# Kernel tuning notes

Measured on AMD Instinct MI355X. Metric: run time of the kernel, lower is better.

## Reference

```python
import jax, jax.numpy as jnp
import numpy as np

N_HEADS = 16


def setup_inputs() -> dict:
    key = jax.random.key(0)
    ks = jax.random.split(key, 4)
    B, S, E = 4, 2048, 1024
    x = jax.random.normal(ks[0], (B, S, E), dtype=jnp.float32)
    w_attn = jax.random.normal(ks[1], (E, 3 * E), dtype=jnp.float32) * 0.02
    b_attn = jnp.zeros((3 * E,), dtype=jnp.float32)
    w_proj = jax.random.normal(ks[2], (E, E), dtype=jnp.float32) * 0.02
    b_proj = jnp.zeros((E,), dtype=jnp.float32)
    return {"x": x, "w_attn": w_attn, "b_attn": b_attn, "w_proj": w_proj, "b_proj": b_proj}


def reference(x, w_attn, b_attn, w_proj, b_proj):
    B, S, E = x.shape
    H = N_HEADS
    D = E // H
    # fused QKV projection (Conv1D: x @ W + b)
    qkv = x @ w_attn + b_attn                     # [B, S, 3E]
    q, k, v = jnp.split(qkv, 3, axis=-1)          # each [B, S, E]
    q = q.reshape(B, S, H, D).transpose(0, 2, 1, 3)  # [B, H, S, D]
    k = k.reshape(B, S, H, D).transpose(0, 2, 1, 3)
    v = v.reshape(B, S, H, D).transpose(0, 2, 1, 3)
    # scaled QK^T
    scores = jnp.einsum('bhqd,bhkd->bhqk', q, k) / jnp.sqrt(jnp.asarray(D, dtype=x.dtype))
    # causal mask via where with dtype-min fill (matches torch.where(c_m, w, finfo.min))
    causal = jnp.tril(jnp.ones((S, S), dtype=bool))  # [S, S]
    scores = jnp.where(causal[None, None, :, :], scores, jnp.finfo(scores.dtype).min)
    attn = jax.nn.softmax(scores, axis=-1)        # [B, H, S, S]
    o = jnp.einsum('bhqk,bhkd->bhqd', attn, v)    # [B, H, S, D]
    o = o.transpose(0, 2, 1, 3).reshape(B, S, E)  # merge heads
    return o @ w_proj + b_proj                    # output projection
```

## Files before the change

kernel.cpp:

```cpp
#include <hip/hip_runtime.h>
#include <stdint.h>


typedef __bf16 bf16;
typedef __bf16 bf16x4 __attribute__((ext_vector_type(4)));
typedef __bf16 bf16x8 __attribute__((ext_vector_type(8)));
typedef float  f32x4  __attribute__((ext_vector_type(4)));

#define DEV __device__ __forceinline__

DEV void async_copy16(bf16* lds, const bf16* g) {
  __builtin_amdgcn_global_load_lds(
      (__attribute__((address_space(1))) void*)(uintptr_t)g,
      (__attribute__((address_space(3))) void*)(uint32_t)(uintptr_t)lds,
      16, 0, 0);
}

__global__ __launch_bounds__(256) void cast_x_kernel(const float* __restrict__ in,
                                                     bf16* __restrict__ out, int n4) {
  int i = blockIdx.x * blockDim.x + threadIdx.x;
  int stride = gridDim.x * blockDim.x;
  for (; i < n4; i += stride) {
    float4 v = ((const float4*)in)[i];
    bf16x4 o = { (bf16)v.x, (bf16)v.y, (bf16)v.z, (bf16)v.w };
    *(bf16x4*)(out + (size_t)i * 4) = o;
  }
}

__global__ __launch_bounds__(256) void transpose_cast_kernel(const float* __restrict__ W,
                                                             bf16* __restrict__ Wt,
                                                             int Kd, int Nd) {
  __shared__ alignas(16) bf16 T[64 * 80];
  const int t = threadIdx.x;
  const int n0 = blockIdx.x * 64;
  const int k0 = blockIdx.y * 64;
#pragma unroll
  for (int i = 0; i < 4; ++i) {
    int idx = t + i * 256;
    int r  = idx >> 4;
    int c4 = (idx & 15) * 4;
    float4 v = *(const float4*)(W + (size_t)(k0 + r) * Nd + n0 + c4);
    bf16x4 o = { (bf16)v.x, (bf16)v.y, (bf16)v.z, (bf16)v.w };
    *(bf16x4*)(&T[r * 80 + c4]) = o;
  }
  __syncthreads();
#pragma unroll
  for (int i = 0; i < 2; ++i) {
    int idx = t + i * 256;
    int n = idx >> 3;
    int c = idx & 7;
    bf16x8 o;
#pragma unroll
    for (int j = 0; j < 8; ++j) o[j] = T[(c * 8 + j) * 80 + n];
    *(bf16x8*)(Wt + (size_t)(n0 + n) * Kd + k0 + c * 8) = o;
  }
}

template <typename OutT, bool FUSE_VT>
__global__ __launch_bounds__(512, 4) void gemm256_kernel(const bf16* __restrict__ A,
                                                         const bf16* __restrict__ Bt,
                                                         const float* __restrict__ bias,
                                                         OutT* __restrict__ C,
                                                         bf16* __restrict__ vtout,
                                                         int M, int N, int K,
                                                         float qscale, int qcols,
                                                         int nbx) {
  __shared__ alignas(16) char smem[73728];
  auto As = (bf16(*)[256 * 32])smem;
  auto Bs = (bf16(*)[128 * 32])(smem + 49152);

  const int tid  = threadIdx.x;
  const int lane = tid & 63;
  const int w    = tid >> 6;
  const int wm = w >> 1, wn = w & 1;
  const int l15 = lane & 15, l16 = lane >> 4;

  const int nwg = (int)gridDim.x;
  const int cpx = nwg >> 3;
  const int swz = ((int)blockIdx.x & 7) * cpx + ((int)blockIdx.x >> 3);
  const int m0 = (swz / nbx) * 256;
  const int n0 = (swz % nbx) * 128;

  const int c0  = w * 64 + lane;
  const int rA0 = c0 >> 2, sA0 = c0 & 3;
  const int rA1 = rA0 + 128;
  const bf16* srcA0 = A  + (size_t)(m0 + rA0) * K + 8 * (sA0 ^ ((rA0 >> 1) & 3));
  const bf16* srcA1 = A  + (size_t)(m0 + rA1) * K + 8 * (sA0 ^ ((rA1 >> 1) & 3));
  const bf16* srcB  = Bt + (size_t)(n0 + rA0) * K + 8 * (sA0 ^ ((rA0 >> 1) & 3));

#define STAGE_TILE(buf, kt)                                       \
  {                                                               \
    const int k0_ = (kt) * 32;                                    \
    async_copy16(&As[buf][(w * 64) * 8],         srcA0 + k0_);    \
    async_copy16(&As[buf][(512 + w * 64) * 8],   srcA1 + k0_);    \
    async_copy16(&Bs[buf][(w * 64) * 8],         srcB  + k0_);    \
  }

  f32x4 acc[4][4];
  f32x4 zf = {0.f, 0.f, 0.f, 0.f};
#pragma unroll
  for (int i = 0; i < 4; ++i)
#pragma unroll
    for (int j = 0; j < 4; ++j) acc[i][j] = zf;

  const int KT = K >> 5;
  STAGE_TILE(0, 0)
  STAGE_TILE(1, 1)

  const int soff = 8 * (l16 ^ ((l15 >> 1) & 3));

  int bufc = 0;
  int bufs = 2;
  for (int kt = 0; kt < KT; ++kt) {
    if (kt < KT - 1) { asm volatile("s_waitcnt vmcnt(3)" ::: "memory"); }
    else             { asm volatile("s_waitcnt vmcnt(0)" ::: "memory"); }
    __builtin_amdgcn_s_barrier();
    asm volatile("" ::: "memory");
    if (kt + 2 < KT) STAGE_TILE(bufs, kt + 2)

    bf16x8 bfr[4], afr[4];
#pragma unroll
    for (int n = 0; n < 4; ++n) {
      int rb = wn * 64 + n * 16 + l15;
      bfr[n] = *(const bf16x8*)(&Bs[bufc][rb * 32 + soff]);
    }
#pragma unroll
    for (int m = 0; m < 4; ++m) {
      int ra = wm * 64 + m * 16 + l15;
      afr[m] = *(const bf16x8*)(&As[bufc][ra * 32 + soff]);
    }
    __builtin_amdgcn_s_setprio(1);
#pragma unroll
    for (int m = 0; m < 4; ++m)
#pragma unroll
      for (int n = 0; n < 4; ++n)
        acc[m][n] = __builtin_amdgcn_mfma_f32_16x16x32_bf16(afr[m], bfr[n], acc[m][n], 0, 0, 0);
    __builtin_amdgcn_s_setprio(0);
    asm volatile("" ::: "memory");
    bufc = (bufc == 2) ? 0 : bufc + 1;
    bufs = (bufs == 2) ? 0 : bufs + 1;
  }

  if (FUSE_VT && n0 >= 2048) {
    __syncthreads();
    bf16* T = (bf16*)smem;
#pragma unroll
    for (int n = 0; n < 4; ++n) {
      int c = wn * 64 + n * 16 + l15;
      float bb = bias[n0 + c];
#pragma unroll
      for (int m = 0; m < 4; ++m) {
        int r0_ = wm * 64 + m * 16 + l16 * 4;
        int key0 = r0_ & 63;
        int pos0 = (key0 & 32) | (((key0 >> 2) & 3) << 3) | (((key0 >> 4) & 1) << 2);
        int rp = (r0_ & ~63) | pos0;
        bf16x4 q = { (bf16)(acc[m][n][0] + bb), (bf16)(acc[m][n][1] + bb),
                     (bf16)(acc[m][n][2] + bb), (bf16)(acc[m][n][3] + bb) };
        *(bf16x4*)(&T[c * 264 + rp]) = q;
      }
    }
    __syncthreads();
    const int b_  = m0 >> 11;
    const int s0_ = m0 & 2047;
    const int ck  = tid & 31;
#pragma unroll
    for (int pass = 0; pass < 8; ++pass) {
      int c = pass * 16 + (tid >> 5);
      int colg = n0 + c - 2048;
      int hh = colg >> 6, d = colg & 63;
      bf16x8 v = *(const bf16x8*)(&T[c * 264 + ck * 8]);
      *(bf16x8*)(vtout + ((size_t)(b_ * 16 + hh) * 64 + d) * 2048 + s0_ + ck * 8) = v;
    }
    return;
  }
#pragma unroll
  for (int n = 0; n < 4; ++n) {
    int col = n0 + wn * 64 + n * 16 + l15;
    float bb = bias[col];
    float sc2 = (col < qcols) ? qscale : 1.0f;
#pragma unroll
    for (int m = 0; m < 4; ++m) {
#pragma unroll
      for (int reg = 0; reg < 4; ++reg) {
        int row = m0 + wm * 64 + m * 16 + l16 * 4 + reg;
        C[(size_t)row * N + col] = (OutT)((acc[m][n][reg] + bb) * sc2);
      }
    }
  }
#undef STAGE_TILE
}

template <typename OutT>
__global__ __launch_bounds__(256, 4) void gemm128_kernel(const bf16* __restrict__ A,
                                                         const bf16* __restrict__ Bt,
                                                         const float* __restrict__ bias,
                                                         OutT* __restrict__ C,
                                                         int M, int N, int K,
                                                         int nbx) {
  __shared__ alignas(16) char smem[49152];
  auto As = (bf16(*)[128 * 32])smem;
  auto Bs = (bf16(*)[128 * 32])(smem + 24576);

  const int tid  = threadIdx.x;
  const int lane = tid & 63;
  const int w    = tid >> 6;
  const int wm = w >> 1, wn = w & 1;
  const int l15 = lane & 15, l16 = lane >> 4;

  const int nwg = (int)gridDim.x;
  const int cpx = nwg >> 3;
  const int swz = ((int)blockIdx.x & 7) * cpx + ((int)blockIdx.x >> 3);
  const int m0 = (swz / nbx) * 128;
  const int n0 = (swz % nbx) * 128;

  const int r0_ = tid >> 2, s0c = tid & 3;
  const int r1_ = r0_ + 64;
  const bf16* srcA0 = A  + (size_t)(m0 + r0_) * K + 8 * (s0c ^ ((r0_ >> 1) & 3));
  const bf16* srcA1 = A  + (size_t)(m0 + r1_) * K + 8 * (s0c ^ ((r1_ >> 1) & 3));
  const bf16* srcB0 = Bt + (size_t)(n0 + r0_) * K + 8 * (s0c ^ ((r0_ >> 1) & 3));
  const bf16* srcB1 = Bt + (size_t)(n0 + r1_) * K + 8 * (s0c ^ ((r1_ >> 1) & 3));

#define STAGE_TILE(buf, kt)                                         \
  {                                                                 \
    const int k0_ = (kt) * 32;                                      \
    async_copy16(&As[buf][(w * 64) * 8],         srcA0 + k0_);      \
    async_copy16(&As[buf][(256 + w * 64) * 8],   srcA1 + k0_);      \
    async_copy16(&Bs[buf][(w * 64) * 8],         srcB0 + k0_);      \
    async_copy16(&Bs[buf][(256 + w * 64) * 8],   srcB1 + k0_);      \
  }

  f32x4 acc[4][4];
  f32x4 zf = {0.f, 0.f, 0.f, 0.f};
#pragma unroll
  for (int i = 0; i < 4; ++i)
#pragma unroll
    for (int j = 0; j < 4; ++j) acc[i][j] = zf;

  const int KT = K >> 5;
  STAGE_TILE(0, 0)
  STAGE_TILE(1, 1)

  const int soff = 8 * (l16 ^ ((l15 >> 1) & 3));

  int bufc = 0;
  int bufs = 2;
  for (int kt = 0; kt < KT; ++kt) {
    if (kt < KT - 1) { asm volatile("s_waitcnt vmcnt(4)" ::: "memory"); }
    else             { asm volatile("s_waitcnt vmcnt(0)" ::: "memory"); }
    __builtin_amdgcn_s_barrier();
    asm volatile("" ::: "memory");
    if (kt + 2 < KT) STAGE_TILE(bufs, kt + 2)

    bf16x8 bfr[4], afr[4];
#pragma unroll
    for (int n = 0; n < 4; ++n) {
      int rb = wn * 64 + n * 16 + l15;
      bfr[n] = *(const bf16x8*)(&Bs[bufc][rb * 32 + soff]);
    }
#pragma unroll
    for (int m = 0; m < 4; ++m) {
      int ra = wm * 64 + m * 16 + l15;
      afr[m] = *(const bf16x8*)(&As[bufc][ra * 32 + soff]);
    }
    __builtin_amdgcn_s_setprio(1);
#pragma unroll
    for (int m = 0; m < 4; ++m)
#pragma unroll
      for (int n = 0; n < 4; ++n)
        acc[m][n] = __builtin_amdgcn_mfma_f32_16x16x32_bf16(afr[m], bfr[n], acc[m][n], 0, 0, 0);
    __builtin_amdgcn_s_setprio(0);
    asm volatile("" ::: "memory");
    bufc = (bufc == 2) ? 0 : bufc + 1;
    bufs = (bufs == 2) ? 0 : bufs + 1;
  }

#pragma unroll
  for (int n = 0; n < 4; ++n) {
    int col = n0 + wn * 64 + n * 16 + l15;
    float bb = bias[col];
#pragma unroll
    for (int m = 0; m < 4; ++m) {
#pragma unroll
      for (int reg = 0; reg < 4; ++reg) {
        int row = m0 + wm * 64 + m * 16 + l16 * 4 + reg;
        C[(size_t)row * N + col] = (OutT)(acc[m][n][reg] + bb);
      }
    }
  }
#undef STAGE_TILE
}

__global__ __launch_bounds__(512, 4) void flash_kernel(const bf16* __restrict__ qkv,
                                                       const bf16* __restrict__ vt,
                                                       bf16* __restrict__ obuf) {
  constexpr int S = 2048, E3 = 3072;
  __shared__ alignas(16) bf16 Ks[2][64 * 64];
  __shared__ alignas(16) bf16 Vs[2][64 * 64];

  const int tid  = threadIdx.x;
  const int lane = tid & 63;
  const int w    = tid >> 6;
  const int i   = (int)blockIdx.x;
  const int bh  = ((i >> 6) << 3) | (i & 7);
  const int bx  = (i >> 3) & 7;
  const int b = bh >> 4, h = bh & 15;
  const int l15 = lane & 15, l16 = lane >> 4;

  const int sr  = w * 8 + (lane >> 3);
  const int scc = lane & 7;
  const bf16* kstage = qkv + (size_t)(b * S + sr) * E3 + 1024 + h * 64 + 8 * (scc ^ (sr & 7));
  const bf16* vstage = vt + (size_t)(bh * 64 + sr) * S + 8 * (scc ^ (sr & 7));

  const int xsw = l15 & 7;
  const uint32_t rdA = (uint32_t)(l15 * 128 + 16 * (l16 ^ xsw));
  const uint32_t rdB = (uint32_t)(l15 * 128 + 16 * ((4 + l16) ^ xsw));

#define KV_STAGE(buf, kv0_)                                        \
  {                                                                \
    async_copy16(Ks[buf] + w * 512, kstage + (size_t)(kv0_) * E3); \
    async_copy16(Vs[buf] + w * 512, vstage + (kv0_));              \
  }

  for (int half = 0; half < 2; ++half) {
    const int t = half ? (15 - bx) : bx;
    const int q0 = t * 128;
    const int wq0 = q0 + w * 16;
    const int nsteps = 2 * t + 2;

    KV_STAGE(0, 0)

    bf16x8 qf[2];
    {
      const bf16* qbase = qkv + (size_t)(b * S + wq0 + l15) * E3 + h * 64;
#pragma unroll
      for (int dk = 0; dk < 2; ++dk)
        qf[dk] = *(const bf16x8*)(qbase + (dk * 4 + l16) * 8);
    }

    float lstate = 0.f;
    f32x4 oacc[4];
    f32x4 zf = {0.f, 0.f, 0.f, 0.f};
#pragma unroll
    for (int i2 = 0; i2 < 4; ++i2) oacc[i2] = zf;

    __syncthreads();

#define FLASH_STEP(CUR, STEPIDX)                                                  \
    {                                                                             \
      const int kv0 = (STEPIDX) * 64;                                             \
      if ((STEPIDX) + 1 < nsteps) KV_STAGE((CUR) ^ 1, kv0 + 64)                   \
      if (kv0 <= wq0 + 15) {                     \
        f32x4 sv[4];                                                              \
        _Pragma("unroll")                                                         \
        for (int kf = 0; kf < 4; ++kf) sv[kf] = zf;                               \
        __builtin_amdgcn_s_setprio(1);                                            \
        _Pragma("unroll")                                                         \
        for (int kf = 0; kf < 4; ++kf) {                                          \
          bf16x8 k0 = *(const bf16x8*)((const char*)Ks[CUR] + rdA + kf * 2048);   \
          sv[kf] = __builtin_amdgcn_mfma_f32_16x16x32_bf16(k0, qf[0], sv[kf], 0, 0, 0); \
          bf16x8 k1 = *(const bf16x8*)((const char*)Ks[CUR] + rdB + kf * 2048);   \
          sv[kf] = __builtin_amdgcn_mfma_f32_16x16x32_bf16(k1, qf[1], sv[kf], 0, 0, 0); \
        }                                                                         \
        __builtin_amdgcn_s_setprio(0);                                            \
        if (kv0 + 63 > wq0) {     \
          const int qrow_ = wq0 + l15;                                            \
          _Pragma("unroll")                                                       \
          for (int kf = 0; kf < 4; ++kf)                                          \
            _Pragma("unroll")                                                     \
            for (int reg = 0; reg < 4; ++reg) {                                   \
              int key = kv0 + kf * 16 + l16 * 4 + reg;                            \
              if (key > qrow_) sv[kf][reg] = -1e30f;                              \
            }                                                                     \
        }                                                                         \
        float rsum = 0.f;                                                         \
        _Pragma("unroll")                                                         \
        for (int kf = 0; kf < 4; ++kf)                                            \
          _Pragma("unroll")                                                       \
          for (int reg = 0; reg < 4; ++reg) {                                     \
            float p = __builtin_amdgcn_exp2f(sv[kf][reg]);                        \
            sv[kf][reg] = p;                                                      \
            rsum += p;                                                            \
          }                                                                       \
        rsum += __shfl_xor(rsum, 16);                                             \
        rsum += __shfl_xor(rsum, 32);                                             \
        lstate += rsum;                                                           \
             \
        bf16x8 pb[2];                                                             \
        _Pragma("unroll")                                                         \
        for (int kc = 0; kc < 2; ++kc) {                                          \
          bf16x8 tq;                                                              \
          tq[0] = (bf16)sv[2 * kc][0];  tq[1] = (bf16)sv[2 * kc][1];              \
          tq[2] = (bf16)sv[2 * kc][2];  tq[3] = (bf16)sv[2 * kc][3];              \
          tq[4] = (bf16)sv[2 * kc + 1][0]; tq[5] = (bf16)sv[2 * kc + 1][1];       \
          tq[6] = (bf16)sv[2 * kc + 1][2]; tq[7] = (bf16)sv[2 * kc + 1][3];       \
          pb[kc] = tq;                                                            \
        }                                                                         \
        __builtin_amdgcn_s_setprio(1);                                            \
        _Pragma("unroll")                                                         \
        for (int nf = 0; nf < 4; ++nf) {                                          \
          bf16x8 vf0 = *(const bf16x8*)((const char*)Vs[CUR] + rdA + nf * 2048);  \
          oacc[nf] = __builtin_amdgcn_mfma_f32_16x16x32_bf16(vf0, pb[0], oacc[nf], 0, 0, 0); \
          bf16x8 vf1 = *(const bf16x8*)((const char*)Vs[CUR] + rdB + nf * 2048);  \
          oacc[nf] = __builtin_amdgcn_mfma_f32_16x16x32_bf16(vf1, pb[1], oacc[nf], 0, 0, 0); \
        }                                                                         \
        __builtin_amdgcn_s_setprio(0);                                            \
      }                                                                           \
      __syncthreads();          \
    }

    for (int step = 0; step < nsteps; step += 2) {
      FLASH_STEP(0, step)
      FLASH_STEP(1, step + 1)
    }
#undef FLASH_STEP

    float inv = 1.0f / lstate;
    int qrow = wq0 + l15;
#pragma unroll
    for (int nf = 0; nf < 4; ++nf) {
      bf16x4 o4 = { (bf16)(oacc[nf][0] * inv), (bf16)(oacc[nf][1] * inv),
                    (bf16)(oacc[nf][2] * inv), (bf16)(oacc[nf][3] * inv) };
      *(bf16x4*)(obuf + (size_t)(b * S + qrow) * 1024 + h * 64 + nf * 16 + l16 * 4) = o4;
    }
  }
#undef KV_STAGE
}

extern "C" void kernel_launch(void* const* d_in, const int* in_sizes, int n_in,
                              void* d_out, int out_size, void* d_ws, size_t ws_size,
                              hipStream_t stream) {
  (void)in_sizes; (void)n_in; (void)out_size; (void)ws_size;
  const float* x      = (const float*)d_in[0];
  const float* w_attn = (const float*)d_in[1];
  const float* b_attn = (const float*)d_in[2];
  const float* w_proj = (const float*)d_in[3];
  const float* b_proj = (const float*)d_in[4];
  float* out = (float*)d_out;

  char* ws = (char*)d_ws;
  bf16* xb  = (bf16*)(ws + 0);
  bf16* wat = (bf16*)(ws + 16777216);
  bf16* wpt = (bf16*)(ws + 23068672);
  bf16* qkv = (bf16*)(ws + 25165824);
  bf16* vt  = (bf16*)(ws + 75497472);
  bf16* ob  = (bf16*)(ws + 92274688);

  const float QSCALE = 0.18033688011112042f;

  cast_x_kernel<<<2048, 256, 0, stream>>>(x, xb, 8192 * 1024 / 4);
  transpose_cast_kernel<<<dim3(48, 16), 256, 0, stream>>>(w_attn, wat, 1024, 3072);
  transpose_cast_kernel<<<dim3(16, 16), 256, 0, stream>>>(w_proj, wpt, 1024, 1024);
  gemm256_kernel<bf16, true><<<768, 512, 0, stream>>>(xb, wat, b_attn, qkv, vt,
                                                      8192, 3072, 1024, QSCALE, 1024, 24);
  flash_kernel<<<512, 512, 0, stream>>>(qkv, vt, ob);
  gemm128_kernel<float><<<512, 256, 0, stream>>>(ob, wpt, b_proj, out,
                                                 8192, 1024, 1024, 8);
}
```

Measured before the change: 146.3 us.

## Switch flash attention to 32x32x16 MFMA with split-KV warp pairs

The flash kernel now uses 32x32x16 bf16 MFMA tiles instead of 16x16x32. Each pair of waves shares a 32-row query block, and each wave of the pair handles one 32-key half of every 64-key tile. The two partial outputs and row sums are combined through new LDS buffers after an extra barrier. The V-transpose permutation in the QKV GEMM epilogue is changed to match the new P register layout expected by the larger MFMA. The aim is fewer MFMA issues and LDS fragment loads per FLOP. In exchange, LDS use rises by about 33 KB and a reduction step is added, which may lower occupancy at 4 blocks per CU.

```diff
diff --git a/kernel.cpp b/kernel.cpp
--- a/kernel.cpp
+++ b/kernel.cpp
@@ -6,6 +6,7 @@
 typedef __bf16 bf16x4 __attribute__((ext_vector_type(4)));
 typedef __bf16 bf16x8 __attribute__((ext_vector_type(8)));
 typedef float  f32x4  __attribute__((ext_vector_type(4)));
+typedef float  f32x16 __attribute__((ext_vector_type(16)));
 
 #define DEV __device__ __forceinline__
 
@@ -152,7 +153,7 @@
       for (int m = 0; m < 4; ++m) {
         int r0_ = wm * 64 + m * 16 + l16 * 4;
         int key0 = r0_ & 63;
-        int pos0 = (key0 & 32) | (((key0 >> 2) & 3) << 3) | (((key0 >> 4) & 1) << 2);
+        int pos0 = (key0 & 0x30) | ((key0 & 8) >> 1) | ((key0 & 4) << 1);
         int rp = (r0_ & ~63) | pos0;
         bf16x4 q = { (bf16)(acc[m][n][0] + bb), (bf16)(acc[m][n][1] + bb),
                      (bf16)(acc[m][n][2] + bb), (bf16)(acc[m][n][3] + bb) };
@@ -296,24 +297,37 @@
   constexpr int S = 2048, E3 = 3072;
   __shared__ alignas(16) bf16 Ks[2][64 * 64];
   __shared__ alignas(16) bf16 Vs[2][64 * 64];
+  __shared__ alignas(16) float Ms[4][32][64];
+  __shared__ float Ls[4][32];
 
   const int tid  = threadIdx.x;
   const int lane = tid & 63;
   const int w    = tid >> 6;
+  const int qg = w >> 1, kh = w & 1;
   const int i   = (int)blockIdx.x;
   const int bh  = ((i >> 6) << 3) | (i & 7);
   const int bx  = (i >> 3) & 7;
   const int b = bh >> 4, h = bh & 15;
-  const int l15 = lane & 15, l16 = lane >> 4;
+  const int l31 = lane & 31, l5 = lane >> 5;
 
   const int sr  = w * 8 + (lane >> 3);
   const int scc = lane & 7;
   const bf16* kstage = qkv + (size_t)(b * S + sr) * E3 + 1024 + h * 64 + 8 * (scc ^ (sr & 7));
   const bf16* vstage = vt + (size_t)(bh * 64 + sr) * S + 8 * (scc ^ (sr & 7));
 
-  const int xsw = l15 & 7;
-  const uint32_t rdA = (uint32_t)(l15 * 128 + 16 * (l16 ^ xsw));
-  const uint32_t rdB = (uint32_t)(l15 * 128 + 16 * ((4 + l16) ^ xsw));
+  const int rK = kh * 32 + l31;
+  uint32_t offK[4];
+#pragma unroll
+  for (int dm = 0; dm < 4; ++dm)
+    offK[dm] = (uint32_t)(rK * 128 + 16 * (((dm << 1) | l5) ^ (rK & 7)));
+  uint32_t offV[2][2];
+#pragma unroll
+  for (int bd = 0; bd < 2; ++bd)
+#pragma unroll
+    for (int kk = 0; kk < 2; ++kk) {
+      int rV = bd * 32 + l31;
+      offV[bd][kk] = (uint32_t)(rV * 128 + 16 * (((kh << 2) | (kk << 1) | l5) ^ (rV & 7)));
+    }
 
 #define KV_STAGE(buf, kv0_)                                        \
   {                                                                \
@@ -321,27 +335,29 @@
     async_copy16(Vs[buf] + w * 512, vstage + (kv0_));              \
   }
 
+  const f32x16 z16 = {0.f,0.f,0.f,0.f,0.f,0.f,0.f,0.f,
+                      0.f,0.f,0.f,0.f,0.f,0.f,0.f,0.f};
+
   for (int half = 0; half < 2; ++half) {
     const int t = half ? (15 - bx) : bx;
     const int q0 = t * 128;
-    const int wq0 = q0 + w * 16;
+    const int wq0 = q0 + qg * 32;
+    const int qrow = wq0 + l31;
     const int nsteps = 2 * t + 2;
 
     KV_STAGE(0, 0)
 
-    bf16x8 qf[2];
+    bf16x8 qf[4];
     {
-      const bf16* qbase = qkv + (size_t)(b * S + wq0 + l15) * E3 + h * 64;
-#pragma unroll
-      for (int dk = 0; dk < 2; ++dk)
-        qf[dk] = *(const bf16x8*)(qbase + (dk * 4 + l16) * 8);
+      const bf16* qbase = qkv + (size_t)(b * S + qrow) * E3 + h * 64 + l5 * 8;
+#pragma unroll
+      for (int mf = 0; mf < 4; ++mf)
+        qf[mf] = *(const bf16x8*)(qbase + mf * 16);
     }
 
     float lstate = 0.f;
-    f32x4 oacc[4];
-    f32x4 zf = {0.f, 0.f, 0.f, 0.f};
-#pragma unroll
-    for (int i2 = 0; i2 < 4; ++i2) oacc[i2] = zf;
+    f32x16 oacc[2];
+    oacc[0] = z16; oacc[1] = z16;
 
     __syncthreads();
 
@@ -349,60 +365,47 @@
     {                                                                             \
       const int kv0 = (STEPIDX) * 64;                                             \
       if ((STEPIDX) + 1 < nsteps) KV_STAGE((CUR) ^ 1, kv0 + 64)                   \
-      if (kv0 <= wq0 + 15) {                     \
-        f32x4 sv[4];                                                              \
-        _Pragma("unroll")                                                         \
-        for (int kf = 0; kf < 4; ++kf) sv[kf] = zf;                               \
+      if (kv0 + kh * 32 <= wq0 + 31) {           \
+        f32x16 sv = z16;                                                          \
         __builtin_amdgcn_s_setprio(1);                                            \
         _Pragma("unroll")                                                         \
-        for (int kf = 0; kf < 4; ++kf) {                                          \
-          bf16x8 k0 = *(const bf16x8*)((const char*)Ks[CUR] + rdA + kf * 2048);   \
-          sv[kf] = __builtin_amdgcn_mfma_f32_16x16x32_bf16(k0, qf[0], sv[kf], 0, 0, 0); \
-          bf16x8 k1 = *(const bf16x8*)((const char*)Ks[CUR] + rdB + kf * 2048);   \
-          sv[kf] = __builtin_amdgcn_mfma_f32_16x16x32_bf16(k1, qf[1], sv[kf], 0, 0, 0); \
+        for (int dm = 0; dm < 4; ++dm) {                                          \
+          bf16x8 kfr = *(const bf16x8*)((const char*)Ks[CUR] + offK[dm]);         \
+          sv = __builtin_amdgcn_mfma_f32_32x32x16_bf16(kfr, qf[dm], sv, 0, 0, 0); \
         }                                                                         \
         __builtin_amdgcn_s_setprio(0);                                            \
-        if (kv0 + 63 > wq0) {     \
-          const int qrow_ = wq0 + l15;                                            \
+        if (kv0 + kh * 32 + 31 > wq0) {          \
           _Pragma("unroll")                                                       \
-          for (int kf = 0; kf < 4; ++kf)                                          \
-            _Pragma("unroll")                                                     \
-            for (int reg = 0; reg < 4; ++reg) {                                   \
-              int key = kv0 + kf * 16 + l16 * 4 + reg;                            \
-              if (key > qrow_) sv[kf][reg] = -1e30f;                              \
-            }                                                                     \
+          for (int r = 0; r < 16; ++r) {                                          \
+            int key = kv0 + kh * 32 + (r & 3) + 8 * (r >> 2) + 4 * l5;            \
+            if (key > qrow) sv[r] = -1e30f;                                       \
+          }                                                                       \
         }                                                                         \
         float rsum = 0.f;                                                         \
         _Pragma("unroll")                                                         \
-        for (int kf = 0; kf < 4; ++kf)                                            \
-          _Pragma("unroll")                                                       \
-          for (int reg = 0; reg < 4; ++reg) {                                     \
-            float p = __builtin_amdgcn_exp2f(sv[kf][reg]);                        \
-            sv[kf][reg] = p;                                                      \
-            rsum += p;                                                            \
-          }                                                                       \
-        rsum += __shfl_xor(rsum, 16);                                             \
+        for (int r = 0; r < 16; ++r) {                                            \
+          float p = __builtin_amdgcn_exp2f(sv[r]);                                \
+          sv[r] = p;                                                              \
+          rsum += p;                                                              \
+        }                                                                         \
         rsum += __shfl_xor(rsum, 32);                                             \
         lstate += rsum;                                                           \
-             \
         bf16x8 pb[2];                                                             \
         _Pragma("unroll")                                                         \
-        for (int kc = 0; kc < 2; ++kc) {                                          \
+        for (int kk = 0; kk < 2; ++kk) {                                          \
           bf16x8 tq;                                                              \
-          tq[0] = (bf16)sv[2 * kc][0];  tq[1] = (bf16)sv[2 * kc][1];              \
-          tq[2] = (bf16)sv[2 * kc][2];  tq[3] = (bf16)sv[2 * kc][3];              \
-          tq[4] = (bf16)sv[2 * kc + 1][0]; tq[5] = (bf16)sv[2 * kc + 1][1];       \
-          tq[6] = (bf16)sv[2 * kc + 1][2]; tq[7] = (bf16)sv[2 * kc + 1][3];       \
-          pb[kc] = tq;                                                            \
+          _Pragma("unroll")                                                       \
+          for (int j = 0; j < 8; ++j) tq[j] = (bf16)sv[kk * 8 + j];               \
+          pb[kk] = tq;                                                            \
         }                                                                         \
         __builtin_amdgcn_s_setprio(1);                                            \
         _Pragma("unroll")                                                         \
-        for (int nf = 0; nf < 4; ++nf) {                                          \
-          bf16x8 vf0 = *(const bf16x8*)((const char*)Vs[CUR] + rdA + nf * 2048);  \
-          oacc[nf] = __builtin_amdgcn_mfma_f32_16x16x32_bf16(vf0, pb[0], oacc[nf], 0, 0, 0); \
-          bf16x8 vf1 = *(const bf16x8*)((const char*)Vs[CUR] + rdB + nf * 2048);  \
-          oacc[nf] = __builtin_amdgcn_mfma_f32_16x16x32_bf16(vf1, pb[1], oacc[nf], 0, 0, 0); \
-        }                                                                         \
+        for (int bd = 0; bd < 2; ++bd)                                            \
+          _Pragma("unroll")                                                       \
+          for (int kk = 0; kk < 2; ++kk) {                                        \
+            bf16x8 vf = *(const bf16x8*)((const char*)Vs[CUR] + offV[bd][kk]);    \
+            oacc[bd] = __builtin_amdgcn_mfma_f32_32x32x16_bf16(vf, pb[kk], oacc[bd], 0, 0, 0); \
+          }                                                                       \
         __builtin_amdgcn_s_setprio(0);                                            \
       }                                                                           \
       __syncthreads();          \
@@ -414,13 +417,31 @@
     }
 #undef FLASH_STEP
 
-    float inv = 1.0f / lstate;
-    int qrow = wq0 + l15;
-#pragma unroll
-    for (int nf = 0; nf < 4; ++nf) {
-      bf16x4 o4 = { (bf16)(oacc[nf][0] * inv), (bf16)(oacc[nf][1] * inv),
-                    (bf16)(oacc[nf][2] * inv), (bf16)(oacc[nf][3] * inv) };
-      *(bf16x4*)(obuf + (size_t)(b * S + qrow) * 1024 + h * 64 + nf * 16 + l16 * 4) = o4;
+    if (kh == 1) {
+#pragma unroll
+      for (int bd = 0; bd < 2; ++bd)
+#pragma unroll
+        for (int r4 = 0; r4 < 4; ++r4) {
+          float4 q4 = { oacc[bd][r4 * 4 + 0], oacc[bd][r4 * 4 + 1],
+                        oacc[bd][r4 * 4 + 2], oacc[bd][r4 * 4 + 3] };
+          *(float4*)(&Ms[qg][l31][bd * 32 + 8 * r4 + 4 * l5]) = q4;
+        }
+      if (l5 == 0) Ls[qg][l31] = lstate;
+    }
+    __syncthreads();
+    if (kh == 0) {
+      float inv = 1.0f / (lstate + Ls[qg][l31]);
+#pragma unroll
+      for (int bd = 0; bd < 2; ++bd)
+#pragma unroll
+        for (int r4 = 0; r4 < 4; ++r4) {
+          float4 p4 = *(const float4*)(&Ms[qg][l31][bd * 32 + 8 * r4 + 4 * l5]);
+          bf16x4 o4 = { (bf16)((oacc[bd][r4 * 4 + 0] + p4.x) * inv),
+                        (bf16)((oacc[bd][r4 * 4 + 1] + p4.y) * inv),
+                        (bf16)((oacc[bd][r4 * 4 + 2] + p4.z) * inv),
+                        (bf16)((oacc[bd][r4 * 4 + 3] + p4.w) * inv) };
+          *(bf16x4*)(obuf + (size_t)(b * S + qrow) * 1024 + h * 64 + bd * 32 + 8 * r4 + 4 * l5) = o4;
+        }
     }
   }
 #undef KV_STAGE
```

Result: no change. 146.8 us (+0.3%).
